# Optimization experiments

Hardware: AMD Instinct MI355X
Metric: run time of the kernel (lower is better)

Reference implementation:

```python
import jax, jax.numpy as jnp
import numpy as np

C_IN = 64
C_HIDDEN = 8
NO_HEADS = 8
INF = 1.0e9
EPS_ATT = 1.0e-10
LN_EPS = 1.0e-5
N_SEQ = 2048
N_RES = 384


def setup_inputs() -> dict:
    key = jax.random.key(0)
    ks = jax.random.split(key, 8)
    HC = NO_HEADS * C_HIDDEN
    m = jax.random.normal(ks[0], (N_SEQ, N_RES, C_IN), dtype=jnp.float32)
    mask = jnp.ones((N_SEQ, N_RES), dtype=jnp.float32)
    s = 0.05
    return {
        "m": m,
        "mask": mask,
        "ln_w": jnp.ones((C_IN,), jnp.float32),
        "ln_b": jnp.zeros((C_IN,), jnp.float32),
        "wq": jax.random.normal(ks[1], (C_IN, HC), jnp.float32) * s,
        "wk": jax.random.normal(ks[2], (C_IN, C_HIDDEN), jnp.float32) * s,
        "wv": jax.random.normal(ks[3], (C_IN, C_HIDDEN), jnp.float32) * s,
        "wg": jax.random.normal(ks[4], (C_IN, HC), jnp.float32) * s,
        "bg": jnp.ones((HC,), jnp.float32),  # gating bias init = 1
        "wo": jax.random.normal(ks[5], (HC, C_IN), jnp.float32) * s,
        "bo": jnp.zeros((C_IN,), jnp.float32),
    }


def reference(m, mask, ln_w, ln_b, wq, wk, wv, wg, bg, wo, bo):
    H, Ch = NO_HEADS, C_HIDDEN
    # transpose: m -> [R, S, C], mask -> [R, S]
    mt = jnp.swapaxes(m, -2, -3)
    mk = jnp.swapaxes(mask, -1, -2)
    # LayerNorm over c_in (population variance, as torch)
    mu = jnp.mean(mt, axis=-1, keepdims=True)
    var = jnp.mean(jnp.square(mt - mu), axis=-1, keepdims=True)
    x = (mt - mu) * jax.lax.rsqrt(var + LN_EPS) * ln_w + ln_b  # [R, S, C]
    # mean-pooled global query over the sequence (MSA depth) dim
    q = jnp.sum(x * mk[..., None], axis=-2) / (jnp.sum(mk, axis=-1)[..., None] + EPS_ATT)  # [R, C]
    q = (q @ wq) * (Ch ** -0.5)
    q = q.reshape(q.shape[:-1] + (H, Ch))  # [R, H, Ch]
    k = x @ wk  # [R, S, Ch] (shared across heads)
    v = x @ wv  # [R, S, Ch]
    a = jnp.einsum("rhc,rsc->rhs", q, k) + (INF * (mk - 1.0))[..., None, :]
    a = jax.nn.softmax(a, axis=-1)  # [R, H, S]
    o = jnp.einsum("rhs,rsc->rhc", a, v)  # [R, H, Ch]
    g = jax.nn.sigmoid(x @ wg + bg).reshape(x.shape[:-1] + (H, Ch))  # [R, S, H, Ch]
    o = o[..., None, :, :] * g  # [R, S, H, Ch]
    o = o.reshape(o.shape[:-2] + (H * Ch,))
    out = o @ wo + bo  # [R, S, C]
    return jnp.swapaxes(out, -2, -3)  # back to [S, R, C]
```

## Files before the change

### kernel.cpp

```cpp
#include <hip/hip_runtime.h>
#include <hip/hip_bf16.h>

#define S_SEQ 2048
#define R_RES 384
#define CIN   64
#define HC    64
#define NH    8
#define CHD   8

using bf16x8 = __attribute__((ext_vector_type(8))) short;
using f32x4  = __attribute__((ext_vector_type(4))) float;

__device__ __forceinline__ short f2bf(float v) {
  __hip_bfloat16 h = __float2bfloat16(v);
  union { __hip_bfloat16 b; short s; } u; u.b = h; return u.s;
}
__device__ __forceinline__ float bf2f(short s) {
  union { short s; __hip_bfloat16 b; } u; u.s = s; return __bfloat162float(u.b);
}

__global__ __launch_bounds__(256) void k0_prep(
    const float* __restrict__ wg, const float* __restrict__ wo,
    const float* __restrict__ wk, const float* __restrict__ wv,
    const float* __restrict__ ln_w, const float* __restrict__ ln_b,
    short* __restrict__ wgT_hi, short* __restrict__ wgT_lo,
    short* __restrict__ woT_hi, short* __restrict__ woT_lo,
    short* __restrict__ wkvT_hi, short* __restrict__ wkvT_lo,
    float* __restrict__ bkv) {
  const int idx = blockIdx.x * 256 + threadIdx.x;
  if (idx < 16) {
    float s = 0.f;
    for (int c = 0; c < CIN; ++c)
      s += ln_b[c] * ((idx < 8) ? wk[c * CHD + idx] : wv[c * CHD + (idx - 8)]);
    bkv[idx] = s;
  }
  if (idx < 16 * CIN) {
    const int a = idx >> 6, c = idx & 63;
    const float w = ln_w[c] * ((a < 8) ? wk[c * CHD + a] : wv[c * CHD + (a - 8)]);
    short h = f2bf(w);
    wkvT_hi[idx] = h; wkvT_lo[idx] = f2bf(w - bf2f(h));
  }
  if (idx >= HC * CIN) return;
  const int a = idx >> 6;
  const int b = idx & 63;
  const float g = wg[b * HC + a];
  short gh = f2bf(g);
  wgT_hi[idx] = gh; wgT_lo[idx] = f2bf(g - bf2f(gh));
  const float o = wo[b * CIN + a];
  short oh = f2bf(o);
  woT_hi[idx] = oh; woT_lo[idx] = f2bf(o - bf2f(oh));
}

__global__ __launch_bounds__(256, 4) void k1_mfma(
    const float* __restrict__ m, const float* __restrict__ mask,
    const short* __restrict__ wkvT_hi, const short* __restrict__ wkvT_lo,
    const float* __restrict__ bkv,
    float* __restrict__ Kd, float* __restrict__ Vd,
    float* __restrict__ qpool_part, float* __restrict__ qm_part) {
  const int r = blockIdx.x;
  const int chunk = blockIdx.y;
  const int tid = threadIdx.x;
  const int wave = tid >> 6;
  const int lane = tid & 63;
  const int lrow = lane & 15;
  const int lpart = lane >> 4;
  const int s_base = chunk * 512 + wave * 128;

  __shared__ float redA[4][CIN];
  __shared__ float redM[4];

  bf16x8 kvh[2], kvl[2];
  #pragma unroll
  for (int k = 0; k < 2; ++k) {
    const int idx = lrow * 64 + k * 32 + lpart * 8;
    kvh[k] = *reinterpret_cast<const bf16x8*>(wkvT_hi + idx);
    kvl[k] = *reinterpret_cast<const bf16x8*>(wkvT_lo + idx);
  }
  const float4 bkvq = *reinterpret_cast<const float4*>(bkv + lpart * 4);

  float qacc[16];
  #pragma unroll
  for (int e = 0; e < 16; ++e) qacc[e] = 0.f;
  float macc = 0.f;

  for (int t = 0; t < 8; ++t) {
    const int srow = s_base + t * 16 + lrow;
    const float* mrow = m + ((size_t)srow * R_RES + r) * CIN;
    float x0[8], x1[8];
    {
      const float4* p0 = reinterpret_cast<const float4*>(mrow + lpart * 8);
      const float4* p1 = reinterpret_cast<const float4*>(mrow + 32 + lpart * 8);
      float4 a = p0[0], b = p0[1], c = p1[0], d = p1[1];
      x0[0]=a.x; x0[1]=a.y; x0[2]=a.z; x0[3]=a.w; x0[4]=b.x; x0[5]=b.y; x0[6]=b.z; x0[7]=b.w;
      x1[0]=c.x; x1[1]=c.y; x1[2]=c.z; x1[3]=c.w; x1[4]=d.x; x1[5]=d.y; x1[6]=d.z; x1[7]=d.w;
    }
    const float mk = mask[(size_t)srow * R_RES + r];

    float s = 0.f;
    #pragma unroll
    for (int e = 0; e < 8; ++e) s += x0[e] + x1[e];
    s += __shfl_xor(s, 16, 64);
    s += __shfl_xor(s, 32, 64);
    const float mean = s * (1.0f / CIN);
    float vs = 0.f;
    #pragma unroll
    for (int e = 0; e < 8; ++e) {
      float d0 = x0[e] - mean, d1 = x1[e] - mean;
      vs += d0 * d0 + d1 * d1;
    }
    vs += __shfl_xor(vs, 16, 64);
    vs += __shfl_xor(vs, 32, 64);
    const float rstd = rsqrtf(vs * (1.0f / CIN) + 1e-5f);

    bf16x8 ah0, al0, ah1, al1;
    #pragma unroll
    for (int e = 0; e < 8; ++e) {
      const float xh0 = (x0[e] - mean) * rstd;
      const float xh1 = (x1[e] - mean) * rstd;
      qacc[e]     += mk * xh0;
      qacc[8 + e] += mk * xh1;
      short h = f2bf(xh0);
      ah0[e] = h; al0[e] = f2bf(xh0 - bf2f(h));
      h = f2bf(xh1);
      ah1[e] = h; al1[e] = f2bf(xh1 - bf2f(h));
    }
    macc += mk;

    f32x4 a = {0.f, 0.f, 0.f, 0.f};
    a = __builtin_amdgcn_mfma_f32_16x16x32_bf16(kvh[0], ah0, a, 0, 0, 0);
    a = __builtin_amdgcn_mfma_f32_16x16x32_bf16(kvh[1], ah1, a, 0, 0, 0);
    a = __builtin_amdgcn_mfma_f32_16x16x32_bf16(kvl[0], ah0, a, 0, 0, 0);
    a = __builtin_amdgcn_mfma_f32_16x16x32_bf16(kvl[1], ah1, a, 0, 0, 0);
    a = __builtin_amdgcn_mfma_f32_16x16x32_bf16(kvh[0], al0, a, 0, 0, 0);
    a = __builtin_amdgcn_mfma_f32_16x16x32_bf16(kvh[1], al1, a, 0, 0, 0);

    const size_t off = ((size_t)r * S_SEQ + srow) * CHD + (lpart & 1) * 4;
    float* dst = ((lpart & 2) ? Vd : Kd) + off;
    *reinterpret_cast<float4*>(dst) =
        make_float4(a[0] + bkvq.x, a[1] + bkvq.y, a[2] + bkvq.z, a[3] + bkvq.w);
  }

  #pragma unroll
  for (int off = 1; off <= 8; off <<= 1) {
    #pragma unroll
    for (int e = 0; e < 16; ++e) qacc[e] += __shfl_xor(qacc[e], off, 64);
    macc += __shfl_xor(macc, off, 64);
  }
  if (lrow == 0) {
    #pragma unroll
    for (int e = 0; e < 8; ++e) {
      redA[wave][lpart * 8 + e] = qacc[e];
      redA[wave][32 + lpart * 8 + e] = qacc[8 + e];
    }
    if (lpart == 0) redM[wave] = macc;
  }
  __syncthreads();
  if (tid < CIN) {
    const float tot = redA[0][tid] + redA[1][tid] + redA[2][tid] + redA[3][tid];
    qpool_part[((size_t)chunk * R_RES + r) * CIN + tid] = tot;
  }
  if (tid == 0)
    qm_part[chunk * R_RES + r] = redM[0] + redM[1] + redM[2] + redM[3];
}

__global__ __launch_bounds__(256) void k2_attn(
    const float* __restrict__ mask,
    const float* __restrict__ ln_w, const float* __restrict__ ln_b,
    const float* __restrict__ wq,
    const float* __restrict__ qpool_part, const float* __restrict__ qm_part,
    const float* __restrict__ Kd, const float* __restrict__ Vd,
    float* __restrict__ od) {
  const int r = blockIdx.x;
  const int tid = threadIdx.x;
  const int lane = tid & 63;
  const int wave = tid >> 6;

  __shared__ float s_q[HC];
  __shared__ float s_qp[CIN];
  __shared__ float redw[4][CIN];
  __shared__ float dred[4][NH];
  __shared__ float mred[4][NH];

  const float msum_tot = qm_part[0 * R_RES + r] + qm_part[1 * R_RES + r] +
                         qm_part[2 * R_RES + r] + qm_part[3 * R_RES + r];

  if (tid < CIN) {
    float A = 0.f;
    #pragma unroll
    for (int ch = 0; ch < 4; ++ch)
      A += qpool_part[((size_t)ch * R_RES + r) * CIN + tid];
    s_qp[tid] = (ln_w[tid] * A + ln_b[tid] * msum_tot) / (msum_tot + 1e-10f);
  }
  __syncthreads();
  if (tid < HC) {
    float qj = 0.f;
    for (int c = 0; c < CIN; ++c) qj += s_qp[c] * wq[c * HC + tid];
    s_q[tid] = qj * 0.35355339059327373f;
  }
  __syncthreads();

  float mh[NH], dp[NH];
  #pragma unroll
  for (int h = 0; h < NH; ++h) { mh[h] = -1e30f; dp[h] = 0.f; }
  float opart[HC];
  #pragma unroll
  for (int i = 0; i < HC; ++i) opart[i] = 0.f;

  for (int s = tid; s < S_SEQ; s += 256) {
    float kk[CHD], vv[CHD];
    const float4* kp = reinterpret_cast<const float4*>(Kd + ((size_t)r * S_SEQ + s) * CHD);
    const float4* vp = reinterpret_cast<const float4*>(Vd + ((size_t)r * S_SEQ + s) * CHD);
    float4 a = kp[0], b = kp[1], c4 = vp[0], d4 = vp[1];
    kk[0] = a.x; kk[1] = a.y; kk[2] = a.z; kk[3] = a.w;
    kk[4] = b.x; kk[5] = b.y; kk[6] = b.z; kk[7] = b.w;
    vv[0] = c4.x; vv[1] = c4.y; vv[2] = c4.z; vv[3] = c4.w;
    vv[4] = d4.x; vv[5] = d4.y; vv[6] = d4.z; vv[7] = d4.w;
    const float madd = 1e9f * (mask[(size_t)s * R_RES + r] - 1.0f);
    #pragma unroll
    for (int h = 0; h < NH; ++h) {
      float l = madd;
      #pragma unroll
      for (int j = 0; j < CHD; ++j) l += s_q[h * CHD + j] * kk[j];
      const float newm = fmaxf(mh[h], l);
      const float sc = __expf(mh[h] - newm);
      const float p  = __expf(l - newm);
      dp[h] = dp[h] * sc + p;
      #pragma unroll
      for (int j = 0; j < CHD; ++j)
        opart[h * CHD + j] = opart[h * CHD + j] * sc + p * vv[j];
      mh[h] = newm;
    }
  }

  float wm[NH];
  #pragma unroll
  for (int h = 0; h < NH; ++h) {
    wm[h] = mh[h];
    #pragma unroll
    for (int off = 32; off >= 1; off >>= 1)
      wm[h] = fmaxf(wm[h], __shfl_xor(wm[h], off, 64));
  }
  if (lane == 0) {
    #pragma unroll
    for (int h = 0; h < NH; ++h) mred[wave][h] = wm[h];
  }
  __syncthreads();
  #pragma unroll
  for (int h = 0; h < NH; ++h)
    wm[h] = fmaxf(fmaxf(mred[0][h], mred[1][h]), fmaxf(mred[2][h], mred[3][h]));

  #pragma unroll
  for (int h = 0; h < NH; ++h) {
    const float sc = __expf(mh[h] - wm[h]);
    dp[h] *= sc;
    #pragma unroll
    for (int j = 0; j < CHD; ++j) opart[h * CHD + j] *= sc;
  }

  #pragma unroll
  for (int h = 0; h < NH; ++h) {
    float v = dp[h];
    #pragma unroll
    for (int off = 32; off >= 1; off >>= 1) v += __shfl_xor(v, off, 64);
    dp[h] = v;
  }
  if (lane == 0) {
    #pragma unroll
    for (int h = 0; h < NH; ++h) dred[wave][h] = dp[h];
  }
  float keep = 0.f;
  #pragma unroll
  for (int c = 0; c < HC; ++c) {
    float val = opart[c];
    #pragma unroll
    for (int off = 32; off >= 1; off >>= 1) val += __shfl_xor(val, off, 64);
    if (lane == c) keep = val;
  }
  redw[wave][lane] = keep;
  __syncthreads();
  if (tid < HC) {
    const float tot = redw[0][tid] + redw[1][tid] + redw[2][tid] + redw[3][tid];
    const int h = tid >> 3;
    const float den = dred[0][h] + dred[1][h] + dred[2][h] + dred[3][h];
    od[(size_t)r * HC + tid] = tot / den;
  }
}

__global__ __launch_bounds__(128) void k3_mfma(
    const float* __restrict__ m,
    const float* __restrict__ ln_w, const float* __restrict__ ln_b,
    const short* __restrict__ wgT_hi, const short* __restrict__ wgT_lo,
    const short* __restrict__ woT_hi, const short* __restrict__ woT_lo,
    const float* __restrict__ bg, const float* __restrict__ bo,
    const float* __restrict__ od, float* __restrict__ out) {
  const int tid = threadIdx.x;
  const int wave = tid >> 6;
  const int lane = tid & 63;
  const int lrow = lane & 15;
  const int lpart = lane >> 4;
  const size_t base = (size_t)blockIdx.x * 128 + (size_t)wave * 64;
  const int base_r = (int)(base % R_RES);

  __shared__ float t_lds[2][64 * 64];
  float* tw = t_lds[wave];

  float bgv[4], bov[4];
  #pragma unroll
  for (int n = 0; n < 4; ++n) { bgv[n] = bg[n * 16 + lrow]; bov[n] = bo[n * 16 + lrow]; }

  float lw0[8], lb0[8], lw1[8], lb1[8];
  {
    const float4* w0 = reinterpret_cast<const float4*>(ln_w + lpart * 8);
    const float4* w1 = reinterpret_cast<const float4*>(ln_w + 32 + lpart * 8);
    const float4* b0 = reinterpret_cast<const float4*>(ln_b + lpart * 8);
    const float4* b1 = reinterpret_cast<const float4*>(ln_b + 32 + lpart * 8);
    float4 a = w0[0], b = w0[1], c = w1[0], d = w1[1];
    lw0[0]=a.x; lw0[1]=a.y; lw0[2]=a.z; lw0[3]=a.w; lw0[4]=b.x; lw0[5]=b.y; lw0[6]=b.z; lw0[7]=b.w;
    lw1[0]=c.x; lw1[1]=c.y; lw1[2]=c.z; lw1[3]=c.w; lw1[4]=d.x; lw1[5]=d.y; lw1[6]=d.z; lw1[7]=d.w;
    a = b0[0]; b = b0[1]; c = b1[0]; d = b1[1];
    lb0[0]=a.x; lb0[1]=a.y; lb0[2]=a.z; lb0[3]=a.w; lb0[4]=b.x; lb0[5]=b.y; lb0[6]=b.z; lb0[7]=b.w;
    lb1[0]=c.x; lb1[1]=c.y; lb1[2]=c.z; lb1[3]=c.w; lb1[4]=d.x; lb1[5]=d.y; lb1[6]=d.z; lb1[7]=d.w;
  }

  bf16x8 b1h[4][2], b1l[4][2];
  #pragma unroll
  for (int n = 0; n < 4; ++n) {
    #pragma unroll
    for (int k = 0; k < 2; ++k) {
      const int idx = (n * 16 + lrow) * 64 + k * 32 + lpart * 8;
      b1h[n][k] = *reinterpret_cast<const bf16x8*>(wgT_hi + idx);
      b1l[n][k] = *reinterpret_cast<const bf16x8*>(wgT_lo + idx);
    }
  }

  #pragma unroll
  for (int mt = 0; mt < 4; ++mt) {
    const size_t grow = base + mt * 16 + lrow;
    const float* mrow = m + grow * CIN;
    float x0[8], x1[8];
    {
      const float4* p0 = reinterpret_cast<const float4*>(mrow + lpart * 8);
      const float4* p1 = reinterpret_cast<const float4*>(mrow + 32 + lpart * 8);
      float4 a = p0[0], b = p0[1], c = p1[0], d = p1[1];
      x0[0]=a.x; x0[1]=a.y; x0[2]=a.z; x0[3]=a.w; x0[4]=b.x; x0[5]=b.y; x0[6]=b.z; x0[7]=b.w;
      x1[0]=c.x; x1[1]=c.y; x1[2]=c.z; x1[3]=c.w; x1[4]=d.x; x1[5]=d.y; x1[6]=d.z; x1[7]=d.w;
    }
    float s = 0.f;
    #pragma unroll
    for (int e = 0; e < 8; ++e) s += x0[e] + x1[e];
    s += __shfl_xor(s, 16, 64);
    s += __shfl_xor(s, 32, 64);
    const float mean = s * (1.0f / CIN);
    float vs = 0.f;
    #pragma unroll
    for (int e = 0; e < 8; ++e) {
      float d0 = x0[e] - mean, d1 = x1[e] - mean;
      vs += d0 * d0 + d1 * d1;
    }
    vs += __shfl_xor(vs, 16, 64);
    vs += __shfl_xor(vs, 32, 64);
    const float rstd = rsqrtf(vs * (1.0f / CIN) + 1e-5f);

    bf16x8 ah0, al0, ah1, al1;
    #pragma unroll
    for (int e = 0; e < 8; ++e) {
      float xn = (x0[e] - mean) * rstd * lw0[e] + lb0[e];
      short h = f2bf(xn);
      ah0[e] = h; al0[e] = f2bf(xn - bf2f(h));
      xn = (x1[e] - mean) * rstd * lw1[e] + lb1[e];
      h = f2bf(xn);
      ah1[e] = h; al1[e] = f2bf(xn - bf2f(h));
    }

    #pragma unroll
    for (int n = 0; n < 4; ++n) {
      f32x4 acc = {0.f, 0.f, 0.f, 0.f};
      acc = __builtin_amdgcn_mfma_f32_16x16x32_bf16(ah0, b1h[n][0], acc, 0, 0, 0);
      acc = __builtin_amdgcn_mfma_f32_16x16x32_bf16(ah1, b1h[n][1], acc, 0, 0, 0);
      acc = __builtin_amdgcn_mfma_f32_16x16x32_bf16(ah0, b1l[n][0], acc, 0, 0, 0);
      acc = __builtin_amdgcn_mfma_f32_16x16x32_bf16(ah1, b1l[n][1], acc, 0, 0, 0);
      acc = __builtin_amdgcn_mfma_f32_16x16x32_bf16(al0, b1h[n][0], acc, 0, 0, 0);
      acc = __builtin_amdgcn_mfma_f32_16x16x32_bf16(al1, b1h[n][1], acc, 0, 0, 0);
      const int j = n * 16 + lrow;
      #pragma unroll
      for (int i = 0; i < 4; ++i) {
        const int rl = mt * 16 + lpart * 4 + i;
        int r = base_r + rl; if (r >= R_RES) r -= R_RES;
        const float z = acc[i] + bgv[n];
        const float g = 1.0f / (1.0f + __expf(-z));
        const float t = g * od[(size_t)r * HC + j];
        const int off = ((rl * 256 + j * 4)) ^ ((rl & 7) << 4);
        *reinterpret_cast<float*>(reinterpret_cast<char*>(tw) + off) = t;
      }
    }
  }

  __syncthreads();

  bf16x8 b2h[4][2], b2l[4][2];
  #pragma unroll
  for (int n = 0; n < 4; ++n) {
    #pragma unroll
    for (int k = 0; k < 2; ++k) {
      const int idx = (n * 16 + lrow) * 64 + k * 32 + lpart * 8;
      b2h[n][k] = *reinterpret_cast<const bf16x8*>(woT_hi + idx);
      b2l[n][k] = *reinterpret_cast<const bf16x8*>(woT_lo + idx);
    }
  }

  #pragma unroll
  for (int mt = 0; mt < 4; ++mt) {
    const int rl2 = mt * 16 + lrow;
    const int swz = (rl2 & 7) << 4;
    bf16x8 ah0, al0, ah1, al1;
    {
      const int a0 = rl2 * 256 + lpart * 32;
      const int a1 = rl2 * 256 + 128 + lpart * 32;
      char* tb = reinterpret_cast<char*>(tw);
      float4 u0 = *reinterpret_cast<float4*>(tb + (a0 ^ swz));
      float4 u1 = *reinterpret_cast<float4*>(tb + ((a0 + 16) ^ swz));
      float4 u2 = *reinterpret_cast<float4*>(tb + (a1 ^ swz));
      float4 u3 = *reinterpret_cast<float4*>(tb + ((a1 + 16) ^ swz));
      float t0[8] = {u0.x, u0.y, u0.z, u0.w, u1.x, u1.y, u1.z, u1.w};
      float t1[8] = {u2.x, u2.y, u2.z, u2.w, u3.x, u3.y, u3.z, u3.w};
      #pragma unroll
      for (int e = 0; e < 8; ++e) {
        short h = f2bf(t0[e]);
        ah0[e] = h; al0[e] = f2bf(t0[e] - bf2f(h));
        h = f2bf(t1[e]);
        ah1[e] = h; al1[e] = f2bf(t1[e] - bf2f(h));
      }
    }
    #pragma unroll
    for (int n = 0; n < 4; ++n) {
      f32x4 acc = {0.f, 0.f, 0.f, 0.f};
      acc = __builtin_amdgcn_mfma_f32_16x16x32_bf16(ah0, b2h[n][0], acc, 0, 0, 0);
      acc = __builtin_amdgcn_mfma_f32_16x16x32_bf16(ah1, b2h[n][1], acc, 0, 0, 0);
      acc = __builtin_amdgcn_mfma_f32_16x16x32_bf16(ah0, b2l[n][0], acc, 0, 0, 0);
      acc = __builtin_amdgcn_mfma_f32_16x16x32_bf16(ah1, b2l[n][1], acc, 0, 0, 0);
      acc = __builtin_amdgcn_mfma_f32_16x16x32_bf16(al0, b2h[n][0], acc, 0, 0, 0);
      acc = __builtin_amdgcn_mfma_f32_16x16x32_bf16(al1, b2h[n][1], acc, 0, 0, 0);
      const int cc = n * 16 + lrow;
      #pragma unroll
      for (int i = 0; i < 4; ++i) {
        const size_t grow = base + mt * 16 + lpart * 4 + i;
        out[grow * CIN + cc] = acc[i] + bov[n];
      }
    }
  }
}

extern "C" void kernel_launch(void* const* d_in, const int* in_sizes, int n_in,
                              void* d_out, int out_size, void* d_ws, size_t ws_size,
                              hipStream_t stream) {
  const float* m    = (const float*)d_in[0];
  const float* mask = (const float*)d_in[1];
  const float* ln_w = (const float*)d_in[2];
  const float* ln_b = (const float*)d_in[3];
  const float* wq   = (const float*)d_in[4];
  const float* wk   = (const float*)d_in[5];
  const float* wv   = (const float*)d_in[6];
  const float* wg   = (const float*)d_in[7];
  const float* bg   = (const float*)d_in[8];
  const float* wo   = (const float*)d_in[9];
  const float* bo   = (const float*)d_in[10];
  float* out = (float*)d_out;

  const size_t sizeK   = (size_t)R_RES * S_SEQ * CHD * sizeof(float);
  const size_t sizeQP  = (size_t)4 * R_RES * CIN * sizeof(float);
  const size_t sizeQM  = (size_t)4 * R_RES * sizeof(float);
  const size_t sizeO   = (size_t)R_RES * HC * sizeof(float);
  const size_t sizeW   = (size_t)HC * CIN * sizeof(short);
  const size_t sizeWKV = (size_t)16 * CIN * sizeof(short);

  char* ws = (char*)d_ws;
  float* Kd         = (float*)(ws);
  float* Vd         = (float*)(ws + sizeK);
  float* qpool_part = (float*)(ws + 2 * sizeK);
  float* qm_part    = (float*)(ws + 2 * sizeK + sizeQP);
  float* od         = (float*)(ws + 2 * sizeK + sizeQP + sizeQM);
  char* wbase       = ws + 2 * sizeK + sizeQP + sizeQM + sizeO;
  short* wgT_hi  = (short*)(wbase);
  short* wgT_lo  = (short*)(wbase + sizeW);
  short* woT_hi  = (short*)(wbase + 2 * sizeW);
  short* woT_lo  = (short*)(wbase + 3 * sizeW);
  short* wkvT_hi = (short*)(wbase + 4 * sizeW);
  short* wkvT_lo = (short*)(wbase + 4 * sizeW + sizeWKV);
  float* bkv     = (float*)(wbase + 4 * sizeW + 2 * sizeWKV);

  k0_prep<<<(HC * CIN + 255) / 256, 256, 0, stream>>>(
      wg, wo, wk, wv, ln_w, ln_b,
      wgT_hi, wgT_lo, woT_hi, woT_lo, wkvT_hi, wkvT_lo, bkv);

  k1_mfma<<<dim3(R_RES, 4), 256, 0, stream>>>(
      m, mask, wkvT_hi, wkvT_lo, bkv, Kd, Vd, qpool_part, qm_part);

  k2_attn<<<R_RES, 256, 0, stream>>>(
      mask, ln_w, ln_b, wq, qpool_part, qm_part, Kd, Vd, od);

  k3_mfma<<<(S_SEQ * R_RES) / 128, 128, 0, stream>>>(
      m, ln_w, ln_b, wgT_hi, wgT_lo, woT_hi, woT_lo, bg, bo, od, out);
}
```

Measured before the change: 219.3 us.

## Split attention over sequence chunks with flash-style combine and separate q prep

```diff
diff --git a/kernel.cpp b/kernel.cpp
--- a/kernel.cpp
+++ b/kernel.cpp
@@ -51,7 +51,7 @@
   woT_hi[idx] = oh; woT_lo[idx] = f2bf(o - bf2f(oh));
 }
 
-__global__ __launch_bounds__(256, 4) void k1_mfma(
+__global__ __launch_bounds__(256) void k1_mfma(
     const float* __restrict__ m, const float* __restrict__ mask,
     const short* __restrict__ wkvT_hi, const short* __restrict__ wkvT_lo,
     const float* __restrict__ bkv,
@@ -163,40 +163,50 @@
     qm_part[chunk * R_RES + r] = redM[0] + redM[1] + redM[2] + redM[3];
 }
 
-__global__ __launch_bounds__(256) void k2_attn(
-    const float* __restrict__ mask,
+__global__ __launch_bounds__(256) void k2q_prep(
     const float* __restrict__ ln_w, const float* __restrict__ ln_b,
     const float* __restrict__ wq,
     const float* __restrict__ qpool_part, const float* __restrict__ qm_part,
+    float* __restrict__ qv) {
+  const int tid = threadIdx.x;
+  const int wave = tid >> 6;
+  const int j = tid & 63;
+  const int r = blockIdx.x * 4 + wave;
+
+  __shared__ float s_qp[4][CIN];
+
+  const float msum_tot = qm_part[0 * R_RES + r] + qm_part[1 * R_RES + r] +
+                         qm_part[2 * R_RES + r] + qm_part[3 * R_RES + r];
+  float A = 0.f;
+  #pragma unroll
+  for (int ch = 0; ch < 4; ++ch)
+    A += qpool_part[((size_t)ch * R_RES + r) * CIN + j];
+  s_qp[wave][j] = (ln_w[j] * A + ln_b[j] * msum_tot) / (msum_tot + 1e-10f);
+  __syncthreads();
+
+  float qj = 0.f;
+  for (int c = 0; c < CIN; ++c) qj += s_qp[wave][c] * wq[c * HC + j];
+  qv[(size_t)r * HC + j] = qj * 0.35355339059327373f;
+}
+
+__global__ __launch_bounds__(256) void k2a_attn_part(
+    const float* __restrict__ mask, const float* __restrict__ qv,
     const float* __restrict__ Kd, const float* __restrict__ Vd,
-    float* __restrict__ od) {
+    float* __restrict__ odp, float* __restrict__ mpart,
+    float* __restrict__ dpart) {
   const int r = blockIdx.x;
+  const int chunk = blockIdx.y;
   const int tid = threadIdx.x;
   const int lane = tid & 63;
   const int wave = tid >> 6;
+  const int s_lo = chunk * 512;
 
   __shared__ float s_q[HC];
-  __shared__ float s_qp[CIN];
   __shared__ float redw[4][CIN];
   __shared__ float dred[4][NH];
   __shared__ float mred[4][NH];
 
-  const float msum_tot = qm_part[0 * R_RES + r] + qm_part[1 * R_RES + r] +
-                         qm_part[2 * R_RES + r] + qm_part[3 * R_RES + r];
-
-  if (tid < CIN) {
-    float A = 0.f;
-    #pragma unroll
-    for (int ch = 0; ch < 4; ++ch)
-      A += qpool_part[((size_t)ch * R_RES + r) * CIN + tid];
-    s_qp[tid] = (ln_w[tid] * A + ln_b[tid] * msum_tot) / (msum_tot + 1e-10f);
-  }
-  __syncthreads();
-  if (tid < HC) {
-    float qj = 0.f;
-    for (int c = 0; c < CIN; ++c) qj += s_qp[c] * wq[c * HC + tid];
-    s_q[tid] = qj * 0.35355339059327373f;
-  }
+  if (tid < HC) s_q[tid] = qv[(size_t)r * HC + tid];
   __syncthreads();
 
   float mh[NH], dp[NH];
@@ -206,7 +216,7 @@
   #pragma unroll
   for (int i = 0; i < HC; ++i) opart[i] = 0.f;
 
-  for (int s = tid; s < S_SEQ; s += 256) {
+  for (int s = s_lo + tid; s < s_lo + 512; s += 256) {
     float kk[CHD], vv[CHD];
     const float4* kp = reinterpret_cast<const float4*>(Kd + ((size_t)r * S_SEQ + s) * CHD);
     const float4* vp = reinterpret_cast<const float4*>(Vd + ((size_t)r * S_SEQ + s) * CHD);
@@ -279,11 +289,39 @@
   redw[wave][lane] = keep;
   __syncthreads();
   if (tid < HC) {
-    const float tot = redw[0][tid] + redw[1][tid] + redw[2][tid] + redw[3][tid];
-    const int h = tid >> 3;
-    const float den = dred[0][h] + dred[1][h] + dred[2][h] + dred[3][h];
-    od[(size_t)r * HC + tid] = tot / den;
-  }
+    odp[((size_t)chunk * R_RES + r) * HC + tid] =
+        redw[0][tid] + redw[1][tid] + redw[2][tid] + redw[3][tid];
+  }
+  if (tid < NH) {
+    dpart[((size_t)chunk * R_RES + r) * NH + tid] =
+        dred[0][tid] + dred[1][tid] + dred[2][tid] + dred[3][tid];
+    mpart[((size_t)chunk * R_RES + r) * NH + tid] = wm[tid];
+  }
+}
+
+__global__ __launch_bounds__(256) void k2b_combine(
+    const float* __restrict__ odp, const float* __restrict__ mpart,
+    const float* __restrict__ dpart, float* __restrict__ od) {
+  const int tid = threadIdx.x;
+  const int r = blockIdx.x * 4 + (tid >> 6);
+  const int j = tid & 63;
+  const int h = j >> 3;
+  float mc[4], dc[4], oc[4];
+  #pragma unroll
+  for (int c = 0; c < 4; ++c) {
+    mc[c] = mpart[((size_t)c * R_RES + r) * NH + h];
+    dc[c] = dpart[((size_t)c * R_RES + r) * NH + h];
+    oc[c] = odp[((size_t)c * R_RES + r) * HC + j];
+  }
+  const float mstar = fmaxf(fmaxf(mc[0], mc[1]), fmaxf(mc[2], mc[3]));
+  float num = 0.f, den = 0.f;
+  #pragma unroll
+  for (int c = 0; c < 4; ++c) {
+    const float sc = __expf(mc[c] - mstar);
+    num += oc[c] * sc;
+    den += dc[c] * sc;
+  }
+  od[(size_t)r * HC + j] = num / den;
 }
 
 __global__ __launch_bounds__(128) void k3_mfma(
@@ -469,6 +507,9 @@
   const size_t sizeK   = (size_t)R_RES * S_SEQ * CHD * sizeof(float);
   const size_t sizeQP  = (size_t)4 * R_RES * CIN * sizeof(float);
   const size_t sizeQM  = (size_t)4 * R_RES * sizeof(float);
+  const size_t sizeQV  = (size_t)R_RES * HC * sizeof(float);
+  const size_t sizeODP = (size_t)4 * R_RES * HC * sizeof(float);
+  const size_t sizeMP  = (size_t)4 * R_RES * NH * sizeof(float);
   const size_t sizeO   = (size_t)R_RES * HC * sizeof(float);
   const size_t sizeW   = (size_t)HC * CIN * sizeof(short);
   const size_t sizeWKV = (size_t)16 * CIN * sizeof(short);
@@ -476,17 +517,21 @@
   char* ws = (char*)d_ws;
   float* Kd         = (float*)(ws);
   float* Vd         = (float*)(ws + sizeK);
-  float* qpool_part = (float*)(ws + 2 * sizeK);
-  float* qm_part    = (float*)(ws + 2 * sizeK + sizeQP);
-  float* od         = (float*)(ws + 2 * sizeK + sizeQP + sizeQM);
-  char* wbase       = ws + 2 * sizeK + sizeQP + sizeQM + sizeO;
-  short* wgT_hi  = (short*)(wbase);
-  short* wgT_lo  = (short*)(wbase + sizeW);
-  short* woT_hi  = (short*)(wbase + 2 * sizeW);
-  short* woT_lo  = (short*)(wbase + 3 * sizeW);
-  short* wkvT_hi = (short*)(wbase + 4 * sizeW);
-  short* wkvT_lo = (short*)(wbase + 4 * sizeW + sizeWKV);
-  float* bkv     = (float*)(wbase + 4 * sizeW + 2 * sizeWKV);
+  char* p           = ws + 2 * sizeK;
+  float* qpool_part = (float*)p;  p += sizeQP;
+  float* qm_part    = (float*)p;  p += sizeQM;
+  float* qv         = (float*)p;  p += sizeQV;
+  float* odp        = (float*)p;  p += sizeODP;
+  float* mpart      = (float*)p;  p += sizeMP;
+  float* dpart      = (float*)p;  p += sizeMP;
+  float* od         = (float*)p;  p += sizeO;
+  short* wgT_hi  = (short*)p;     p += sizeW;
+  short* wgT_lo  = (short*)p;     p += sizeW;
+  short* woT_hi  = (short*)p;     p += sizeW;
+  short* woT_lo  = (short*)p;     p += sizeW;
+  short* wkvT_hi = (short*)p;     p += sizeWKV;
+  short* wkvT_lo = (short*)p;     p += sizeWKV;
+  float* bkv     = (float*)p;
 
   k0_prep<<<(HC * CIN + 255) / 256, 256, 0, stream>>>(
       wg, wo, wk, wv, ln_w, ln_b,
@@ -495,8 +540,13 @@
   k1_mfma<<<dim3(R_RES, 4), 256, 0, stream>>>(
       m, mask, wkvT_hi, wkvT_lo, bkv, Kd, Vd, qpool_part, qm_part);
 
-  k2_attn<<<R_RES, 256, 0, stream>>>(
-      mask, ln_w, ln_b, wq, qpool_part, qm_part, Kd, Vd, od);
+  k2q_prep<<<R_RES / 4, 256, 0, stream>>>(
+      ln_w, ln_b, wq, qpool_part, qm_part, qv);
+
+  k2a_attn_part<<<dim3(R_RES, 4), 256, 0, stream>>>(
+      mask, qv, Kd, Vd, odp, mpart, dpart);
+
+  k2b_combine<<<R_RES / 4, 256, 0, stream>>>(odp, mpart, dpart, od);
 
   k3_mfma<<<(S_SEQ * R_RES) / 128, 128, 0, stream>>>(
       m, ln_w, ln_b, wgT_hi, wgT_lo, woT_hi, woT_lo, bg, bo, od, out);
```

After: 236.9 us. +8.0%, slower.
